# Kernel tuning notes

Hardware: AMD Instinct MI355X
Metric: run time of the kernel (lower is better)

Reference implementation:

```python
import jax, jax.numpy as jnp
import numpy as np

B, N, K, D, H = 4, 8192, 16, 128, 4
DK = D // H  # key_dim = num_hiddens // num_heads
NEG_INF = -1e9


def setup_inputs() -> dict:
    key = jax.random.key(0)
    ks = jax.random.split(key, 16)
    s = 1.0 / np.sqrt(D)
    return {
        "vertex_feat": jax.random.normal(ks[0], (B, N, D), dtype=jnp.float32),
        "neighbors_idx": jax.random.randint(ks[1], (B, N, K), 0, N, dtype=jnp.int32),
        "valid_lens": jax.random.randint(ks[2], (B, N), 0, K, dtype=jnp.int32),
        # MultiHeadAttention projections (keras EinsumDense with bias)
        "Wq": (jax.random.normal(ks[3], (D, H, DK)) * s).astype(jnp.float32),
        "bq": jnp.zeros((H, DK), jnp.float32),
        "Wk": (jax.random.normal(ks[4], (D, H, DK)) * s).astype(jnp.float32),
        "bk": jnp.zeros((H, DK), jnp.float32),
        "Wv": (jax.random.normal(ks[5], (D, H, DK)) * s).astype(jnp.float32),
        "bv": jnp.zeros((H, DK), jnp.float32),
        "Wo": (jax.random.normal(ks[6], (H, DK, D)) * s).astype(jnp.float32),
        "bo": jnp.zeros((D,), jnp.float32),
        # MLP: Dense(D, relu) -> Dense(D)
        "W1": (jax.random.normal(ks[7], (D, D)) * s).astype(jnp.float32),
        "b1": jnp.zeros((D,), jnp.float32),
        "W2": (jax.random.normal(ks[8], (D, D)) * s).astype(jnp.float32),
        "b2": jnp.zeros((D,), jnp.float32),
    }


def reference(vertex_feat, neighbors_idx, valid_lens,
              Wq, bq, Wk, bk, Wv, bv, Wo, bo, W1, b1, W2, b2):
    # query: [B, N, 1, D]; gathered neighbors (batch_dims=1): [B, N, K, D]
    q = vertex_feat[:, :, None, :]
    neigh = jax.vmap(lambda vf, idx: vf[idx])(vertex_feat, neighbors_idx)
    value = jnp.concatenate([q, neigh], axis=2)  # [B, N, K+1, D]

    # per-head projections
    qh = jnp.einsum('bnqd,dhk->bnqhk', q, Wq) + bq      # [B,N,1,H,DK]
    kh = jnp.einsum('bnsd,dhk->bnshk', value, Wk) + bk  # [B,N,K+1,H,DK]
    vh = jnp.einsum('bnsd,dhk->bnshk', value, Wv) + bv

    # attention over the neighbor axis (attention_axes=(2,))
    scores = jnp.einsum('bnqhk,bnshk->bnhqs', qh, kh) / np.sqrt(DK)  # [B,N,H,1,K+1]
    # mask: positions < valid_lens + 1 (self + valid neighbors)
    pos = jnp.arange(K + 1)[None, None, :]                # [1,1,K+1]
    mask = pos < (valid_lens + 1)[:, :, None]             # [B,N,K+1] bool
    scores = scores + jnp.where(mask, 0.0, NEG_INF)[:, :, None, None, :]
    attn = jax.nn.softmax(scores, axis=-1)                # [B,N,H,1,K+1]

    ctx = jnp.einsum('bnhqs,bnshk->bnqhk', attn, vh)      # [B,N,1,H,DK]
    out = jnp.einsum('bnqhk,hkd->bnqd', ctx, Wo) + bo     # [B,N,1,D]
    out = out[:, :, 0, :]                                  # squeeze -> [B,N,D]

    # MLP (dropout inactive at inference)
    h = jax.nn.relu(out @ W1 + b1)
    new_vertex_feat = h @ W2 + b2
    return new_vertex_feat
```

## Files before the change

kernel.cpp:

```cpp
#include <hip/hip_runtime.h>
#include <math.h>

#define BB 4
#define NN 8192
#define KNB 16
#define DD 128
#define SS 17
#define M_TOT (BB*NN)
#define WPAD 136

typedef __attribute__((ext_vector_type(8))) short          bf8;
typedef __attribute__((ext_vector_type(4))) float          f4;
typedef __attribute__((ext_vector_type(4))) unsigned short u16x4;

static __device__ __forceinline__ unsigned short f2bf(float f) {
    unsigned u = __builtin_bit_cast(unsigned, f);
    u += 0x7fffu + ((u >> 16) & 1u);
    return (unsigned short)(u >> 16);
}
static __device__ __forceinline__ float bf2f(unsigned short h) {
    return __builtin_bit_cast(float, (unsigned)h << 16);
}
static __device__ __forceinline__ float bf2f_s(short h) {
    return __builtin_bit_cast(float, (unsigned)(unsigned short)h << 16);
}

__global__ __launch_bounds__(256) void cvt_wT(
    const float* __restrict__ Wq, const float* __restrict__ Wk,
    const float* __restrict__ Wv, const float* __restrict__ Wo,
    const float* __restrict__ W1, const float* __restrict__ W2,
    unsigned short* __restrict__ out)
{
    int m = blockIdx.x >> 4;
    const float* src = (m == 0) ? Wq : (m == 1) ? Wk : (m == 2) ? Wv
                     : (m == 3) ? Wo : (m == 4) ? W1 : W2;
    unsigned short* dst = out + m * 16384;
    int o = (blockIdx.x & 15) * 1024 + threadIdx.x * 4;
    int n = o >> 7, k = o & 127;
    u16x4 r;
    #pragma unroll
    for (int i = 0; i < 4; ++i) r[i] = f2bf(src[(size_t)(k + i) * 128 + n]);
    *(u16x4*)(dst + o) = r;
}

__global__ __launch_bounds__(256) void qkv_kernel(
    const float* __restrict__ X, const unsigned short* __restrict__ WtT,
    const float* __restrict__ bq, const float* __restrict__ bk,
    const float* __restrict__ bv,
    unsigned short* __restrict__ qh, unsigned short* __restrict__ kh,
    unsigned short* __restrict__ vh)
{
    __shared__ unsigned short Xs[64 * WPAD];
    __shared__ unsigned short Wb[128 * WPAD];

    const int tid  = threadIdx.x;
    const int row0 = blockIdx.x * 64;

    {
        const float4* Xg = (const float4*)(X + (size_t)row0 * DD);
        #pragma unroll
        for (int i = 0; i < 8; ++i) {
            int idx = tid + i * 256;
            int r = idx >> 5, c4 = idx & 31;
            float4 v = Xg[idx];
            u16x4 u;
            u[0] = f2bf(v.x); u[1] = f2bf(v.y); u[2] = f2bf(v.z); u[3] = f2bf(v.w);
            *(u16x4*)(Xs + r * WPAD + c4 * 4) = u;
        }
    }
    #pragma unroll
    for (int i = 0; i < 8; ++i) {
        int c = tid + i * 256;
        int n = c >> 4, k8 = c & 15;
        *(bf8*)(Wb + n * WPAD + k8 * 8) = ((const bf8*)WtT)[c];
    }

    const int lane = tid & 63, wv = tid >> 6;
    const int ln = lane & 15, quad = lane >> 4;
    __syncthreads();

    bf8 afr[4];
    #pragma unroll
    for (int s = 0; s < 4; ++s)
        afr[s] = *(const bf8*)(Xs + (wv * 16 + ln) * WPAD + s * 32 + quad * 8);

    const float* biases[3] = { bq, bk, bv };
    unsigned short* outs[3] = { qh, kh, vh };

    #pragma unroll 1
    for (int g = 0; g < 3; ++g) {
        if (g > 0) {
            __syncthreads();
            const bf8* Wn = (const bf8*)(WtT + g * 16384);
            #pragma unroll
            for (int i = 0; i < 8; ++i) {
                int c = tid + i * 256;
                int n = c >> 4, k8 = c & 15;
                *(bf8*)(Wb + n * WPAD + k8 * 8) = Wn[c];
            }
            __syncthreads();
        }

        f4 acc[8] = {};
        #pragma unroll
        for (int t = 0; t < 8; ++t) {
            bf8 bfr[4];
            #pragma unroll
            for (int s = 0; s < 4; ++s)
                bfr[s] = *(const bf8*)(Wb + (t * 16 + ln) * WPAD + s * 32 + quad * 8);
            #pragma unroll
            for (int s = 0; s < 4; ++s)
                acc[t] = __builtin_amdgcn_mfma_f32_16x16x32_bf16(afr[s], bfr[s], acc[t], 0, 0, 0);
        }

        const float* bias = biases[g];
        unsigned short* Y = outs[g];
        #pragma unroll
        for (int t = 0; t < 8; ++t) {
            int col = t * 16 + ln;
            float bc = bias[col];
            #pragma unroll
            for (int r = 0; r < 4; ++r) {
                int row = row0 + wv * 16 + quad * 4 + r;
                Y[(size_t)row * DD + col] = f2bf(acc[t][r] + bc);
            }
        }
    }
}

__global__ __launch_bounds__(256) void attn_kernel(
    const unsigned short* __restrict__ Qh, const unsigned short* __restrict__ Kh,
    const unsigned short* __restrict__ Vh, const int* __restrict__ nbr,
    const int* __restrict__ vlen, unsigned short* __restrict__ Ctx)
{
    const int tid  = threadIdx.x;
    const int vloc = tid >> 4;
    const int ln   = tid & 15;
    const int blk  = blockIdx.x;
    const int b    = (blk & 7) >> 1;
    const int j    = ((blk >> 3) << 1) | (blk & 1);
    const int v    = b * NN + j * 16 + vloc;

    bf8 q8 = *(const bf8*)(Qh + (size_t)v * DD + ln * 8);
    float qf[8];
    #pragma unroll
    for (int i = 0; i < 8; ++i) qf[i] = bf2f_s(q8[i]);

    int rows[SS];
    rows[0] = v;
    {
        const int4* np = (const int4*)(nbr + (size_t)v * KNB);
        #pragma unroll
        for (int i = 0; i < 4; ++i) {
            int4 n4 = np[i];
            rows[1 + i * 4 + 0] = b * NN + n4.x;
            rows[1 + i * 4 + 1] = b * NN + n4.y;
            rows[1 + i * 4 + 2] = b * NN + n4.z;
            rows[1 + i * 4 + 3] = b * NN + n4.w;
        }
    }

    float sc[SS];
    #pragma unroll
    for (int s = 0; s < SS; ++s) {
        bf8 k8 = *(const bf8*)(Kh + (size_t)rows[s] * DD + ln * 8);
        float p = 0.f;
        #pragma unroll
        for (int i = 0; i < 8; ++i) p = fmaf(qf[i], bf2f_s(k8[i]), p);
        p += __shfl_xor(p, 1, 4);
        p += __shfl_xor(p, 2, 4);
        sc[s] = p * 0.17677669529663687f;
    }

    const int len = vlen[v];
    float m = sc[0];
    #pragma unroll
    for (int s = 1; s < SS; ++s) m = (s <= len) ? fmaxf(m, sc[s]) : m;
    float sum = 0.f;
    #pragma unroll
    for (int s = 0; s < SS; ++s) {
        float e = (s <= len) ? __expf(sc[s] - m) : 0.f;
        sc[s] = e;
        sum += e;
    }
    const float inv = 1.f / sum;

    float acc[8] = {};
    #pragma unroll
    for (int s = 0; s < SS; ++s) {
        bf8 v8 = *(const bf8*)(Vh + (size_t)rows[s] * DD + ln * 8);
        float w = sc[s] * inv;
        #pragma unroll
        for (int i = 0; i < 8; ++i) acc[i] = fmaf(w, bf2f_s(v8[i]), acc[i]);
    }
    bf8 r;
    #pragma unroll
    for (int i = 0; i < 8; ++i) r[i] = (short)f2bf(acc[i]);
    *(bf8*)(Ctx + (size_t)v * DD + ln * 8) = r;
}

__global__ __launch_bounds__(256) void ffn_kernel(
    const unsigned short* __restrict__ Ctxg, const unsigned short* __restrict__ WtT3,
    const float* __restrict__ bo, const float* __restrict__ b1,
    const float* __restrict__ b2, float* __restrict__ Out)
{
    __shared__ unsigned short Ct[64 * WPAD];
    __shared__ unsigned short Wb[128 * WPAD];

    const int tid  = threadIdx.x;
    const int row0 = blockIdx.x * 64;

    {
        const bf8* Cg = (const bf8*)(Ctxg + (size_t)row0 * DD);
        #pragma unroll
        for (int i = 0; i < 4; ++i) {
            int idx = tid + i * 256;
            int r = idx >> 4, c8 = idx & 15;
            *(bf8*)(Ct + r * WPAD + c8 * 8) = Cg[idx];
        }
    }
    #pragma unroll
    for (int i = 0; i < 8; ++i) {
        int c = tid + i * 256;
        int n = c >> 4, k8 = c & 15;
        *(bf8*)(Wb + n * WPAD + k8 * 8) = ((const bf8*)WtT3)[c];
    }

    const int lane = tid & 63, wv = tid >> 6;
    const int ln = lane & 15, quad = lane >> 4;
    const float* biases[3] = { bo, b1, b2 };
    __syncthreads();

    #pragma unroll 1
    for (int g = 0; g < 3; ++g) {
        bf8 afr[4];
        #pragma unroll
        for (int s = 0; s < 4; ++s)
            afr[s] = *(const bf8*)(Ct + (wv * 16 + ln) * WPAD + s * 32 + quad * 8);

        f4 acc[8] = {};
        #pragma unroll
        for (int t = 0; t < 8; ++t) {
            bf8 bfr[4];
            #pragma unroll
            for (int s = 0; s < 4; ++s)
                bfr[s] = *(const bf8*)(Wb + (t * 16 + ln) * WPAD + s * 32 + quad * 8);
            #pragma unroll
            for (int s = 0; s < 4; ++s)
                acc[t] = __builtin_amdgcn_mfma_f32_16x16x32_bf16(afr[s], bfr[s], acc[t], 0, 0, 0);
        }

        __syncthreads();

        const float* bias = biases[g];
        if (g == 2) {
            #pragma unroll
            for (int t = 0; t < 8; ++t) {
                int col = t * 16 + ln;
                float bc = bias[col];
                #pragma unroll
                for (int r = 0; r < 4; ++r) {
                    int row = row0 + wv * 16 + quad * 4 + r;
                    Out[(size_t)row * DD + col] = acc[t][r] + bc;
                }
            }
        } else {
            const bf8* Wn = (const bf8*)(WtT3 + (g + 1) * 16384);
            #pragma unroll
            for (int i = 0; i < 8; ++i) {
                int c = tid + i * 256;
                int n = c >> 4, k8 = c & 15;
                *(bf8*)(Wb + n * WPAD + k8 * 8) = Wn[c];
            }
            #pragma unroll
            for (int t = 0; t < 8; ++t) {
                int col = t * 16 + ln;
                float bc = bias[col];
                #pragma unroll
                for (int r = 0; r < 4; ++r) {
                    int rloc = wv * 16 + quad * 4 + r;
                    float vv = acc[t][r] + bc;
                    if (g == 1) vv = fmaxf(vv, 0.f);
                    Ct[rloc * WPAD + col] = f2bf(vv);
                }
            }
            __syncthreads();
        }
    }
}

extern "C" void kernel_launch(void* const* d_in, const int* in_sizes, int n_in,
                              void* d_out, int out_size, void* d_ws, size_t ws_size,
                              hipStream_t stream)
{
    const float* vf   = (const float*)d_in[0];
    const int*   nbr  = (const int*)  d_in[1];
    const int*   vlen = (const int*)  d_in[2];
    const float* Wq   = (const float*)d_in[3];
    const float* bq   = (const float*)d_in[4];
    const float* Wk   = (const float*)d_in[5];
    const float* bk   = (const float*)d_in[6];
    const float* Wv   = (const float*)d_in[7];
    const float* bv   = (const float*)d_in[8];
    const float* Wo   = (const float*)d_in[9];
    const float* bo   = (const float*)d_in[10];
    const float* W1   = (const float*)d_in[11];
    const float* b1   = (const float*)d_in[12];
    const float* W2   = (const float*)d_in[13];
    const float* b2   = (const float*)d_in[14];

    float* out = (float*)d_out;

    const size_t SZ = (size_t)M_TOT * DD;
    unsigned short* WtT = (unsigned short*)d_ws;
    unsigned short* qh  = WtT + 6 * 16384;
    unsigned short* kh  = qh + SZ;
    unsigned short* vh  = kh + SZ;
    unsigned short* ctx = vh + SZ;

    cvt_wT<<<96, 256, 0, stream>>>(Wq, Wk, Wv, Wo, W1, W2, WtT);

    qkv_kernel<<<M_TOT / 64, 256, 0, stream>>>(vf, WtT, bq, bk, bv, qh, kh, vh);

    attn_kernel<<<M_TOT / 16, 256, 0, stream>>>(qh, kh, vh, nbr, vlen, ctx);

    ffn_kernel<<<M_TOT / 64, 256, 0, stream>>>(ctx, WtT + 3 * 16384, bo, b1, b2, out);
}
```

Measured before the change: 132.7 us.

## Interleave K/V rows and skip masked neighbors with online softmax

K and V projections are now stored interleaved in one 256-wide row, so each gathered neighbor brings its key and value from a single contiguous 512-byte row. The attention loop runs only over the valid positions (s <= len) and uses an online softmax, so masked neighbors are never loaded. The cost is a data-dependent loop length, which causes divergence inside a wavefront, plus an extra exp per step and a serial dependency chain in place of independent, fully unrolled loads.

```diff
diff --git a/kernel.cpp b/kernel.cpp
--- a/kernel.cpp
+++ b/kernel.cpp
@@ -8,6 +8,7 @@
 #define SS 17
 #define M_TOT (BB*NN)
 #define WPAD 136
+#define KVS 256
 
 typedef __attribute__((ext_vector_type(8))) short          bf8;
 typedef __attribute__((ext_vector_type(4))) float          f4;
@@ -17,9 +18,6 @@
     unsigned u = __builtin_bit_cast(unsigned, f);
     u += 0x7fffu + ((u >> 16) & 1u);
     return (unsigned short)(u >> 16);
-}
-static __device__ __forceinline__ float bf2f(unsigned short h) {
-    return __builtin_bit_cast(float, (unsigned)h << 16);
 }
 static __device__ __forceinline__ float bf2f_s(short h) {
     return __builtin_bit_cast(float, (unsigned)(unsigned short)h << 16);
@@ -47,8 +45,7 @@
     const float* __restrict__ X, const unsigned short* __restrict__ WtT,
     const float* __restrict__ bq, const float* __restrict__ bk,
     const float* __restrict__ bv,
-    unsigned short* __restrict__ qh, unsigned short* __restrict__ kh,
-    unsigned short* __restrict__ vh)
+    unsigned short* __restrict__ qh, unsigned short* __restrict__ kv)
 {
     __shared__ unsigned short Xs[64 * WPAD];
     __shared__ unsigned short Wb[128 * WPAD];
@@ -84,9 +81,6 @@
     for (int s = 0; s < 4; ++s)
         afr[s] = *(const bf8*)(Xs + (wv * 16 + ln) * WPAD + s * 32 + quad * 8);
 
-    const float* biases[3] = { bq, bk, bv };
-    unsigned short* outs[3] = { qh, kh, vh };
-
     #pragma unroll 1
     for (int g = 0; g < 3; ++g) {
         if (g > 0) {
@@ -113,8 +107,12 @@
                 acc[t] = __builtin_amdgcn_mfma_f32_16x16x32_bf16(afr[s], bfr[s], acc[t], 0, 0, 0);
         }
 
-        const float* bias = biases[g];
-        unsigned short* Y = outs[g];
+        const float* bias = (g == 0) ? bq : (g == 1) ? bk : bv;
+        unsigned short* Y;
+        int ystride;
+        if (g == 0) { Y = qh;       ystride = DD;  }
+        else        { Y = kv + (g == 2 ? 128 : 0); ystride = KVS; }
+
         #pragma unroll
         for (int t = 0; t < 8; ++t) {
             int col = t * 16 + ln;
@@ -122,16 +120,16 @@
             #pragma unroll
             for (int r = 0; r < 4; ++r) {
                 int row = row0 + wv * 16 + quad * 4 + r;
-                Y[(size_t)row * DD + col] = f2bf(acc[t][r] + bc);
+                Y[(size_t)row * ystride + col] = f2bf(acc[t][r] + bc);
             }
         }
     }
 }
 
 __global__ __launch_bounds__(256) void attn_kernel(
-    const unsigned short* __restrict__ Qh, const unsigned short* __restrict__ Kh,
-    const unsigned short* __restrict__ Vh, const int* __restrict__ nbr,
-    const int* __restrict__ vlen, unsigned short* __restrict__ Ctx)
+    const unsigned short* __restrict__ Qh, const unsigned short* __restrict__ KV,
+    const int* __restrict__ nbr, const int* __restrict__ vlen,
+    unsigned short* __restrict__ Ctx)
 {
     const int tid  = threadIdx.x;
     const int vloc = tid >> 4;
@@ -160,42 +158,36 @@
         }
     }
 
-    float sc[SS];
-    #pragma unroll
-    for (int s = 0; s < SS; ++s) {
-        bf8 k8 = *(const bf8*)(Kh + (size_t)rows[s] * DD + ln * 8);
+    const int len = vlen[v];
+
+    float m = -1e30f, l = 0.f;
+    float acc[8] = {};
+    for (int s = 0; s <= len; ++s) {
+        const unsigned short* kvrow = KV + (size_t)rows[s] * KVS;
+        bf8 k8 = *(const bf8*)(kvrow + ln * 8);
+        bf8 v8 = *(const bf8*)(kvrow + 128 + ln * 8);
+
         float p = 0.f;
         #pragma unroll
         for (int i = 0; i < 8; ++i) p = fmaf(qf[i], bf2f_s(k8[i]), p);
         p += __shfl_xor(p, 1, 4);
         p += __shfl_xor(p, 2, 4);
-        sc[s] = p * 0.17677669529663687f;
-    }
-
-    const int len = vlen[v];
-    float m = sc[0];
-    #pragma unroll
-    for (int s = 1; s < SS; ++s) m = (s <= len) ? fmaxf(m, sc[s]) : m;
-    float sum = 0.f;
-    #pragma unroll
-    for (int s = 0; s < SS; ++s) {
-        float e = (s <= len) ? __expf(sc[s] - m) : 0.f;
-        sc[s] = e;
-        sum += e;
-    }
-    const float inv = 1.f / sum;
-
-    float acc[8] = {};
-    #pragma unroll
-    for (int s = 0; s < SS; ++s) {
-        bf8 v8 = *(const bf8*)(Vh + (size_t)rows[s] * DD + ln * 8);
-        float w = sc[s] * inv;
-        #pragma unroll
-        for (int i = 0; i < 8; ++i) acc[i] = fmaf(w, bf2f_s(v8[i]), acc[i]);
-    }
+        p *= 0.17677669529663687f;
+
+        float mn    = fmaxf(m, p);
+        float e     = __expf(p - mn);
+        float scale = __expf(m - mn);
+        l = l * scale + e;
+        #pragma unroll
+        for (int i = 0; i < 8; ++i)
+            acc[i] = fmaf(acc[i], scale, e * bf2f_s(v8[i]));
+        m = mn;
+    }
+
+    const float inv = 1.f / l;
     bf8 r;
     #pragma unroll
-    for (int i = 0; i < 8; ++i) r[i] = (short)f2bf(acc[i]);
+    for (int i = 0; i < 8; ++i) r[i] = (short)f2bf(acc[i] * inv);
     *(bf8*)(Ctx + (size_t)v * DD + ln * 8) = r;
 }
 
@@ -228,7 +220,6 @@
 
     const int lane = tid & 63, wv = tid >> 6;
     const int ln = lane & 15, quad = lane >> 4;
-    const float* biases[3] = { bo, b1, b2 };
     __syncthreads();
 
     #pragma unroll 1
@@ -252,7 +243,7 @@
 
         __syncthreads();
 
-        const float* bias = biases[g];
+        const float* bias = (g == 0) ? bo : (g == 1) ? b1 : b2;
         if (g == 2) {
             #pragma unroll
             for (int t = 0; t < 8; ++t) {
@@ -314,15 +305,14 @@
     const size_t SZ = (size_t)M_TOT * DD;
     unsigned short* WtT = (unsigned short*)d_ws;
     unsigned short* qh  = WtT + 6 * 16384;
-    unsigned short* kh  = qh + SZ;
-    unsigned short* vh  = kh + SZ;
-    unsigned short* ctx = vh + SZ;
+    unsigned short* kv  = qh + SZ;
+    unsigned short* ctx = kv + 2 * SZ;
 
     cvt_wT<<<96, 256, 0, stream>>>(Wq, Wk, Wv, Wo, W1, W2, WtT);
 
-    qkv_kernel<<<M_TOT / 64, 256, 0, stream>>>(vf, WtT, bq, bk, bv, qh, kh, vh);
-
-    attn_kernel<<<M_TOT / 16, 256, 0, stream>>>(qh, kh, vh, nbr, vlen, ctx);
+    qkv_kernel<<<M_TOT / 64, 256, 0, stream>>>(vf, WtT, bq, bk, bv, qh, kv);
+
+    attn_kernel<<<M_TOT / 16, 256, 0, stream>>>(qh, kv, nbr, vlen, ctx);
 
     ffn_kernel<<<M_TOT / 64, 256, 0, stream>>>(ctx, WtT + 3 * 16384, bo, b1, b2, out);
 }
```

New measurement: 136.6 us. 3.0% more time.
